# Kernel tuning notes

Measured on AMD Instinct MI355X. Metric: run time of the kernel, lower is better.

The kernel has to match this reference:

```python
import jax, jax.numpy as jnp
import numpy as np
import math

B = 8
LATENT = 1024
K_DIM = 128   # conv input channels / view dim k
M_DIM = 256   # attention feature dim m
N = 4096      # points_num // num_branch; attention seq len
EPS = 1e-5


def _bn(h, g, b, m, v):
    # inference-mode BatchNorm1d over [B, C, L]
    return (h - m[None, :, None]) * (g / jnp.sqrt(v + EPS))[None, :, None] + b[None, :, None]


def _conv(h, w, b):
    # Conv1d with kernel_size=1 == channel matmul: h [B,C,L], w [O,C]
    return jnp.einsum('bcl,oc->bol', h, w) + b[None, :, None]


def setup_inputs() -> dict:
    key = jax.random.key(0)
    ks = jax.random.split(key, 64)
    it = iter(range(64))

    def nrm(shape, scale=0.05):
        return jax.random.normal(ks[next(it)], shape, jnp.float32) * scale

    def pos(shape):
        return jax.random.uniform(ks[next(it)], shape, jnp.float32, 0.5, 1.5)

    d = {}
    d['x'] = jax.random.normal(ks[next(it)], (B, LATENT), jnp.float32)
    d['fc1_w'] = nrm((M_DIM * K_DIM, LATENT))
    d['fc1_b'] = nrm((M_DIM * K_DIM,))
    d['c1q_w'] = nrm((64, K_DIM)); d['c1q_b'] = nrm((64,))
    d['c2q_w'] = nrm((128, 64));   d['c2q_b'] = nrm((128,))
    d['c3q_w'] = nrm((N, 128));    d['c3q_b'] = nrm((N,))
    d['c3k_w'] = nrm((N, 128));    d['c3k_b'] = nrm((N,))
    d['c1v_w'] = nrm((64, K_DIM)); d['c1v_b'] = nrm((64,))
    d['c2v_w'] = nrm((128, 64));   d['c2v_b'] = nrm((128,))
    d['c3v_w'] = nrm((N, 128));    d['c3v_b'] = nrm((N,))
    for nm, c in [('bn1q', 64), ('bn2q', 128), ('bn1k', 64), ('bn2k', 128), ('bn1v', 64), ('bn2v', 128)]:
        d[nm + '_g'] = pos((c,))
        d[nm + '_be'] = nrm((c,))
        d[nm + '_m'] = nrm((c,))
        d[nm + '_v'] = pos((c,))
    d['co_w'] = nrm((3, M_DIM)); d['co_b'] = nrm((3,))
    return d


def _forward(x, fc1_w, fc1_b, c1q_w, c1q_b, c2q_w, c2q_b, c3q_w, c3q_b, c3k_w, c3k_b,
             c1v_w, c1v_b, c2v_w, c2v_b, c3v_w, c3v_b,
             bn1q_g, bn1q_be, bn1q_m, bn1q_v, bn2q_g, bn2q_be, bn2q_m, bn2q_v,
             bn1k_g, bn1k_be, bn1k_m, bn1k_v, bn2k_g, bn2k_be, bn2k_m, bn2k_v,
             bn1v_g, bn1v_be, bn1v_m, bn1v_v, bn2v_g, bn2v_be, bn2v_m, bn2v_v,
             co_w, co_b):
    h = (x @ fc1_w.T + fc1_b).reshape(-1, M_DIM, K_DIM)   # [B, m, k]
    h = jnp.transpose(h, (0, 2, 1))                        # [B, k, m]
    # Q path
    Q = jax.nn.relu(_bn(_conv(h, c1q_w, c1q_b), bn1q_g, bn1q_be, bn1q_m, bn1q_v))
    Q = jax.nn.relu(_bn(_conv(Q, c2q_w, c2q_b), bn2q_g, bn2q_be, bn2q_m, bn2q_v))
    Q = _conv(Q, c3q_w, c3q_b)                             # [B, n, m]
    # K path: source re-uses conv1_q / conv2_q weights (faithful to original)
    K = jax.nn.relu(_bn(_conv(h, c1q_w, c1q_b), bn1k_g, bn1k_be, bn1k_m, bn1k_v))
    K = jax.nn.relu(_bn(_conv(K, c2q_w, c2q_b), bn2k_g, bn2k_be, bn2k_m, bn2k_v))
    K = _conv(K, c3k_w, c3k_b)                             # [B, n, m]
    # V path
    V = jax.nn.relu(_bn(_conv(h, c1v_w, c1v_b), bn1v_g, bn1v_be, bn1v_m, bn1v_v))
    V = jax.nn.relu(_bn(_conv(V, c2v_w, c2v_b), bn2v_g, bn2v_be, bn2v_m, bn2v_v))
    V = _conv(V, c3v_w, c3v_b)                             # [B, n, m]
    # hand-rolled attention: scores [B, n, n] (source scales by sqrt(k))
    scores = jnp.einsum('bim,bjm->bij', Q, K) / math.sqrt(K_DIM)
    attn = jax.nn.softmax(scores, axis=2)
    out = jnp.einsum('bij,bjm->bim', attn, V)              # [B, n, m]
    out = jnp.einsum('bnm,om->bon', out, co_w) + co_b[None, :, None]  # [B, 3, n]
    return jnp.transpose(out, (0, 2, 1))                   # [B, n, 3]


def reference(x, fc1_w, fc1_b, c1q_w, c1q_b, c2q_w, c2q_b, c3q_w, c3q_b, c3k_w, c3k_b,
              c1v_w, c1v_b, c2v_w, c2v_b, c3v_w, c3v_b,
              bn1q_g, bn1q_be, bn1q_m, bn1q_v, bn2q_g, bn2q_be, bn2q_m, bn2q_v,
              bn1k_g, bn1k_be, bn1k_m, bn1k_v, bn2k_g, bn2k_be, bn2k_m, bn2k_v,
              bn1v_g, bn1v_be, bn1v_m, bn1v_v, bn2v_g, bn2v_be, bn2v_m, bn2v_v,
              co_w, co_b):
    return _forward(x, fc1_w, fc1_b, c1q_w, c1q_b, c2q_w, c2q_b, c3q_w, c3q_b, c3k_w, c3k_b,
                    c1v_w, c1v_b, c2v_w, c2v_b, c3v_w, c3v_b,
                    bn1q_g, bn1q_be, bn1q_m, bn1q_v, bn2q_g, bn2q_be, bn2q_m, bn2q_v,
                    bn1k_g, bn1k_be, bn1k_m, bn1k_v, bn2k_g, bn2k_be, bn2k_m, bn2k_v,
                    bn1v_g, bn1v_be, bn1v_m, bn1v_v, bn2v_g, bn2v_be, bn2v_m, bn2v_v,
                    co_w, co_b)
```

## Files before the change

kernel.cpp:

```cpp
#include <hip/hip_runtime.h>
#include <cstdint>
#include <cstddef>

#define EPS 1e-5f

typedef __attribute__((ext_vector_type(8))) short bf16x8;
typedef __attribute__((ext_vector_type(4))) float f32x4;
typedef __attribute__((ext_vector_type(16))) float f32x16;

__device__ __forceinline__ unsigned short rne_bf16(float f) {
  union { float f; unsigned int u; } v; v.f = f;
  unsigned int u = v.u;
  return (unsigned short)((u + 0x7fffu + ((u >> 16) & 1u)) >> 16);
}
__device__ __forceinline__ float bf16_to_f(unsigned short h) {
  union { unsigned int u; float f; } v; v.u = ((unsigned int)h) << 16; return v.f;
}
__device__ __forceinline__ void split_hl(float v, unsigned short& h, unsigned short& l) {
  h = rne_bf16(v);
  l = rne_bf16(v - bf16_to_f(h));
}
__device__ __forceinline__ f32x4 mfma16(bf16x8 a, bf16x8 b, f32x4 c) {
  return __builtin_amdgcn_mfma_f32_16x16x32_bf16(a, b, c, 0, 0, 0);
}
__device__ __forceinline__ f32x16 mfma32(bf16x8 a, bf16x8 b, f32x16 c) {
  return __builtin_amdgcn_mfma_f32_32x32x16_bf16(a, b, c, 0, 0, 0);
}

__global__ __launch_bounds__(256) void k_fc1(const float* __restrict__ x,
                                             const float* __restrict__ w,
                                             const float* __restrict__ bias,
                                             float* __restrict__ h_t) {
  const int lane = threadIdx.x & 63;
  const int wv = threadIdx.x >> 6;
  const int r = blockIdx.x * 4 + wv;
  const float4* wr = (const float4*)(w + (size_t)r * 1024);
  float acc[8] = {0, 0, 0, 0, 0, 0, 0, 0};
#pragma unroll
  for (int i = 0; i < 4; ++i) {
    float4 wv4 = wr[lane + i * 64];
#pragma unroll
    for (int b = 0; b < 8; ++b) {
      float4 xv = ((const float4*)(x + b * 1024))[lane + i * 64];
      acc[b] += wv4.x * xv.x + wv4.y * xv.y + wv4.z * xv.z + wv4.w * xv.w;
    }
  }
#pragma unroll
  for (int d = 1; d < 64; d <<= 1) {
#pragma unroll
    for (int b = 0; b < 8; ++b) acc[b] += __shfl_xor(acc[b], d);
  }
  if (lane == 0) {
    const int mm = r >> 7, kk = r & 127;
    const float bb = bias[r];
#pragma unroll
    for (int b = 0; b < 8; ++b) h_t[b * 32768 + kk * 256 + mm] = acc[b] + bb;
  }
}

__global__ __launch_bounds__(256) void k_conv1(
    const float* __restrict__ h_t,
    const float* __restrict__ c1q_w, const float* __restrict__ c1q_b,
    const float* __restrict__ c1v_w, const float* __restrict__ c1v_b,
    const float* __restrict__ g1q, const float* __restrict__ be1q,
    const float* __restrict__ mu1q, const float* __restrict__ va1q,
    const float* __restrict__ g1k, const float* __restrict__ be1k,
    const float* __restrict__ mu1k, const float* __restrict__ va1k,
    const float* __restrict__ g1v, const float* __restrict__ be1v,
    const float* __restrict__ mu1v, const float* __restrict__ va1v,
    float* __restrict__ T1q, float* __restrict__ T1k, float* __restrict__ T1v) {
  const int m = threadIdx.x;
  const int o = blockIdx.x & 63;
  const int b = blockIdx.x >> 6;
  const int path = blockIdx.y;
  const float* w = (path == 0 ? c1q_w : c1v_w) + o * 128;
  const float* h = h_t + b * 32768 + m;
  float acc = 0.f;
#pragma unroll 8
  for (int c = 0; c < 128; ++c) acc += w[c] * h[c * 256];
  if (path == 0) {
    const float z = acc + c1q_b[o];
    const float sq = g1q[o] / sqrtf(va1q[o] + EPS);
    T1q[b * 16384 + o * 256 + m] = fmaxf((z - mu1q[o]) * sq + be1q[o], 0.f);
    const float sk = g1k[o] / sqrtf(va1k[o] + EPS);
    T1k[b * 16384 + o * 256 + m] = fmaxf((z - mu1k[o]) * sk + be1k[o], 0.f);
  } else {
    const float z = acc + c1v_b[o];
    const float sv = g1v[o] / sqrtf(va1v[o] + EPS);
    T1v[b * 16384 + o * 256 + m] = fmaxf((z - mu1v[o]) * sv + be1v[o], 0.f);
  }
}

__global__ __launch_bounds__(256) void k_conv2(
    const float* __restrict__ T1q, const float* __restrict__ T1k,
    const float* __restrict__ T1v,
    const float* __restrict__ c2q_w, const float* __restrict__ c2q_b,
    const float* __restrict__ c2v_w, const float* __restrict__ c2v_b,
    const float* __restrict__ g2q, const float* __restrict__ be2q,
    const float* __restrict__ mu2q, const float* __restrict__ va2q,
    const float* __restrict__ g2k, const float* __restrict__ be2k,
    const float* __restrict__ mu2k, const float* __restrict__ va2k,
    const float* __restrict__ g2v, const float* __restrict__ be2v,
    const float* __restrict__ mu2v, const float* __restrict__ va2v,
    unsigned short* __restrict__ Q2H, unsigned short* __restrict__ Q2L,
    unsigned short* __restrict__ K2H, unsigned short* __restrict__ K2L,
    float* __restrict__ V2F) {
  const int m = threadIdx.x;
  const int b = blockIdx.x;
  const int path = blockIdx.y;
  const int oc = blockIdx.z;
  const float* T1 = (path == 0 ? T1q : path == 1 ? T1k : T1v) + b * 16384 + m;
  const float* w = (path == 2 ? c2v_w : c2q_w);
  const float* cb = (path == 2 ? c2v_b : c2q_b);
  const float* g = (path == 0 ? g2q : path == 1 ? g2k : g2v);
  const float* be = (path == 0 ? be2q : path == 1 ? be2k : be2v);
  const float* mu = (path == 0 ? mu2q : path == 1 ? mu2k : mu2v);
  const float* va = (path == 0 ? va2q : path == 1 ? va2k : va2v);
  float t[64];
#pragma unroll
  for (int c = 0; c < 64; ++c) t[c] = T1[c * 256];
  unsigned short* oh =
      (path == 0 ? Q2H : K2H) + b * 32768 + m * 128 + oc * 64;
  unsigned short* ol =
      (path == 0 ? Q2L : K2L) + b * 32768 + m * 128 + oc * 64;
  for (int og = 0; og < 8; ++og) {
    bf16x8 ph, pl;
#pragma unroll
    for (int j = 0; j < 8; ++j) {
      const int o = oc * 64 + og * 8 + j;
      float acc = cb[o];
      const float* wo = w + o * 64;
#pragma unroll
      for (int c = 0; c < 64; ++c) acc += wo[c] * t[c];
      const float s = g[o] / sqrtf(va[o] + EPS);
      const float val = fmaxf((acc - mu[o]) * s + be[o], 0.f);
      if (path == 2) {
        V2F[b * 32768 + o * 256 + m] = val;
      } else {
        unsigned short hh, ll;
        split_hl(val, hh, ll);
        ph[j] = (short)hh; pl[j] = (short)ll;
      }
    }
    if (path != 2) {
      *(bf16x8*)(oh + og * 8) = ph;
      *(bf16x8*)(ol + og * 8) = pl;
    }
  }
}

__global__ __launch_bounds__(256) void k_conv3all(
    const float* __restrict__ c3q_w, const float* __restrict__ c3q_b,
    const float* __restrict__ c3k_w, const float* __restrict__ c3k_b,
    const unsigned short* __restrict__ Q2H, const unsigned short* __restrict__ Q2L,
    const unsigned short* __restrict__ K2H, const unsigned short* __restrict__ K2L,
    unsigned short* __restrict__ QhB, unsigned short* __restrict__ QlB,
    unsigned short* __restrict__ KhB, unsigned short* __restrict__ KlB,
    const float* __restrict__ c3v_w, const float* __restrict__ c3v_b,
    const float* __restrict__ V2F, const float* __restrict__ co_w,
    float4* __restrict__ Vpp) {
  const int z = blockIdx.z;
  const int b = blockIdx.y;
  if (z == 2) {
    if (blockIdx.x >= 16) return;
    __shared__ float Us[387];
    __shared__ float Up[256][3];
    const int tt = threadIdx.x;
    {
      const int c = tt >> 1, mh = tt & 1;
      const float* v = V2F + b * 32768 + c * 256 + mh * 128;
      const float* cw0 = co_w + mh * 128;
      float u0 = 0.f, u1 = 0.f, u2 = 0.f;
#pragma unroll 4
      for (int mm = 0; mm < 128; ++mm) {
        const float xv = v[mm];
        u0 += xv * cw0[mm];
        u1 += xv * cw0[256 + mm];
        u2 += xv * cw0[512 + mm];
      }
      Up[tt][0] = u0; Up[tt][1] = u1; Up[tt][2] = u2;
      if (tt < 3) {
        float s = 0.f;
        for (int mm = 0; mm < 256; ++mm) s += co_w[tt * 256 + mm];
        Us[384 + tt] = s;
      }
    }
    __syncthreads();
    if ((tt & 1) == 0) {
      const int c = tt >> 1;
      Us[c * 3 + 0] = Up[tt][0] + Up[tt + 1][0];
      Us[c * 3 + 1] = Up[tt][1] + Up[tt + 1][1];
      Us[c * 3 + 2] = Up[tt][2] + Up[tt + 1][2];
    }
    __syncthreads();
    const int n = blockIdx.x * 256 + tt;
    const float* w = c3v_w + (size_t)n * 128;
    float a0 = 0.f, a1 = 0.f, a2 = 0.f;
#pragma unroll 4
    for (int c = 0; c < 128; ++c) {
      const float wc = w[c];
      a0 += wc * Us[c * 3 + 0];
      a1 += wc * Us[c * 3 + 1];
      a2 += wc * Us[c * 3 + 2];
    }
    const float bb = c3v_b[n];
    Vpp[(size_t)b * 4096 + n] =
        make_float4(a0 + bb * Us[384], a1 + bb * Us[385], a2 + bb * Us[386], 0.f);
    return;
  }
  const float* W = (z == 0) ? c3q_w : c3k_w;
  const float* bias = (z == 0) ? c3q_b : c3k_b;
  const unsigned short* Xh = (z == 0) ? Q2H : K2H;
  const unsigned short* Xl = (z == 0) ? Q2L : K2L;
  unsigned short* Yh = (z == 0) ? QhB : KhB;
  unsigned short* Yl = (z == 0) ? QlB : KlB;
  const float scale = (z == 0) ? 0.08838834764831845f * 1.4426950408889634f : 1.0f;
  const int lane = threadIdx.x & 63, wv = threadIdx.x >> 6;
  const int l15 = lane & 15, quad = lane >> 4;
  const unsigned short* XH = Xh + b * 32768;
  const unsigned short* XL = Xl + b * 32768;
  unsigned short* YH = Yh + (size_t)b * 4096 * 256;
  unsigned short* YL = Yl + (size_t)b * 4096 * 256;
  const int nb = blockIdx.x * 64 + wv * 16;
  const float* wr = W + (size_t)(nb + l15) * 128 + quad * 8;
  bf16x8 ah[4], al[4];
#pragma unroll
  for (int ks = 0; ks < 4; ++ks) {
#pragma unroll
    for (int j = 0; j < 8; ++j) {
      unsigned short hh, ll;
      split_hl(wr[ks * 32 + j], hh, ll);
      ah[ks][j] = (short)hh; al[ks][j] = (short)ll;
    }
  }
  f32x4 acc[16];
#pragma unroll
  for (int ms = 0; ms < 16; ++ms) acc[ms] = (f32x4){0, 0, 0, 0};
#pragma unroll
  for (int ks = 0; ks < 4; ++ks) {
#pragma unroll
    for (int ms = 0; ms < 16; ++ms) {
      const size_t off = (size_t)(ms * 16 + l15) * 128 + ks * 32 + quad * 8;
      bf16x8 bh = *(const bf16x8*)(XH + off);
      bf16x8 bl = *(const bf16x8*)(XL + off);
      acc[ms] = mfma16(ah[ks], bh, acc[ms]);
      acc[ms] = mfma16(al[ks], bh, acc[ms]);
      acc[ms] = mfma16(ah[ks], bl, acc[ms]);
    }
  }
#pragma unroll
  for (int r = 0; r < 4; ++r) {
    const int n = nb + quad * 4 + r;
    const float bv = bias[n];
#pragma unroll
    for (int ms = 0; ms < 16; ++ms) {
      const float v = (acc[ms][r] + bv) * scale;
      unsigned short hh, ll;
      split_hl(v, hh, ll);
      YH[(size_t)n * 256 + ms * 16 + l15] = hh;
      YL[(size_t)n * 256 + ms * 16 + l15] = ll;
    }
  }
}

__global__ __launch_bounds__(256, 2) void k_attn(
    const unsigned short* __restrict__ Qh, const unsigned short* __restrict__ Ql,
    const unsigned short* __restrict__ Kh, const unsigned short* __restrict__ Kl,
    const float4* __restrict__ Vpp, float4* __restrict__ part) {
  __shared__ __align__(16) short Kt[2][2][32 * 264];
  __shared__ __align__(16) float4 Vt[2][32];
  const int t = threadIdx.x;
  const int lane = t & 63, wv = t >> 6;
  const int l31 = lane & 31, half = lane >> 5;
  const int b = blockIdx.x & 7;
  const int qt = (blockIdx.x >> 3) & 31;
  const int jh = blockIdx.x >> 8;
  const int qrow = qt * 128 + wv * 32 + l31;
  const size_t qoff = ((size_t)b * 4096 + qrow) * 256 + half * 8;
  bf16x8 qfh[16], qfl[16];
#pragma unroll
  for (int kc = 0; kc < 16; ++kc) {
    qfh[kc] = *(const bf16x8*)(Qh + qoff + kc * 16);
    qfl[kc] = *(const bf16x8*)(Ql + qoff + kc * 16);
  }
  const unsigned short* Kgh = Kh + (size_t)b * 4096 * 256;
  const unsigned short* Kgl = Kl + (size_t)b * 4096 * 256;
  const float4* Vg = Vpp + (size_t)b * 4096;
  const int r0 = t >> 5;
  const int sseg = (t & 31) * 8;
  float a0 = 0.f, a1 = 0.f, a2 = 0.f, al = 0.f;
  const int jt0 = jh * 64;
  {
    const int jbase = jt0 * 32;
#pragma unroll
    for (int i = 0; i < 4; ++i) {
      const int row = i * 8 + r0;
      const size_t g = (size_t)(jbase + row) * 256 + sseg;
      *(bf16x8*)&Kt[0][0][row * 264 + sseg] = *(const bf16x8*)(Kgh + g);
      *(bf16x8*)&Kt[0][1][row * 264 + sseg] = *(const bf16x8*)(Kgl + g);
    }
    if (t < 32) Vt[0][t] = Vg[jbase + t];
  }
  __syncthreads();
  for (int it = 0; it < 64; ++it) {
    const int cur = it & 1, nxt = cur ^ 1;
    const bool pf = (it < 63);
    bf16x8 th[4], tl[4];
    float4 vpf = make_float4(0.f, 0.f, 0.f, 0.f);
    if (pf) {
      const int jb2 = (jt0 + it + 1) * 32;
#pragma unroll
      for (int i = 0; i < 4; ++i) {
        const size_t g = (size_t)(jb2 + i * 8 + r0) * 256 + sseg;
        th[i] = *(const bf16x8*)(Kgh + g);
        tl[i] = *(const bf16x8*)(Kgl + g);
      }
      if (t < 32) vpf = Vg[jb2 + t];
    }
    f32x16 sA, sB;
#pragma unroll
    for (int r = 0; r < 16; ++r) { sA[r] = 0.f; sB[r] = 0.f; }
    const short* KH = Kt[cur][0];
    const short* KL = Kt[cur][1];
#pragma unroll
    for (int kc = 0; kc < 16; ++kc) {
      bf16x8 kh = *(const bf16x8*)&KH[l31 * 264 + kc * 16 + half * 8];
      bf16x8 kl = *(const bf16x8*)&KL[l31 * 264 + kc * 16 + half * 8];
      sA = mfma32(kh, qfh[kc], sA);
      sB = mfma32(kh, qfl[kc], sB);
      sA = mfma32(kl, qfh[kc], sA);
    }
#pragma unroll
    for (int r = 0; r < 16; ++r) {
      const float p = __builtin_amdgcn_exp2f(sA[r] + sB[r]);
      const float4 vj = Vt[cur][(r & 3) + 8 * (r >> 2) + 4 * half];
      a0 += p * vj.x; a1 += p * vj.y; a2 += p * vj.z; al += p;
    }
    if (pf) {
#pragma unroll
      for (int i = 0; i < 4; ++i) {
        const int row = i * 8 + r0;
        *(bf16x8*)&Kt[nxt][0][row * 264 + sseg] = th[i];
        *(bf16x8*)&Kt[nxt][1][row * 264 + sseg] = tl[i];
      }
      if (t < 32) Vt[nxt][t] = vpf;
    }
    __syncthreads();
  }
  a0 += __shfl_xor(a0, 32);
  a1 += __shfl_xor(a1, 32);
  a2 += __shfl_xor(a2, 32);
  al += __shfl_xor(al, 32);
  if (half == 0)
    part[(size_t)jh * 32768 + (size_t)b * 4096 + qrow] =
        make_float4(a0, a1, a2, al);
}

__global__ __launch_bounds__(256) void k_combine(
    const float4* __restrict__ part, const float* __restrict__ co_b,
    float* __restrict__ out) {
  const int i = blockIdx.x * 256 + threadIdx.x;
  const float4 pa = part[i];
  const float4 pb = part[32768 + i];
  const float rl = 1.f / (pa.w + pb.w);
  const float b0 = co_b[0], b1 = co_b[1], b2 = co_b[2];
  out[(size_t)i * 3 + 0] = (pa.x + pb.x) * rl + b0;
  out[(size_t)i * 3 + 1] = (pa.y + pb.y) * rl + b1;
  out[(size_t)i * 3 + 2] = (pa.z + pb.z) * rl + b2;
}

extern "C" void kernel_launch(void* const* d_in, const int* in_sizes, int n_in,
                              void* d_out, int out_size, void* d_ws, size_t ws_size,
                              hipStream_t stream) {
  const float* x = (const float*)d_in[0];
  const float* fc1_w = (const float*)d_in[1];
  const float* fc1_b = (const float*)d_in[2];
  const float* c1q_w = (const float*)d_in[3];
  const float* c1q_b = (const float*)d_in[4];
  const float* c2q_w = (const float*)d_in[5];
  const float* c2q_b = (const float*)d_in[6];
  const float* c3q_w = (const float*)d_in[7];
  const float* c3q_b = (const float*)d_in[8];
  const float* c3k_w = (const float*)d_in[9];
  const float* c3k_b = (const float*)d_in[10];
  const float* c1v_w = (const float*)d_in[11];
  const float* c1v_b = (const float*)d_in[12];
  const float* c2v_w = (const float*)d_in[13];
  const float* c2v_b = (const float*)d_in[14];
  const float* c3v_w = (const float*)d_in[15];
  const float* c3v_b = (const float*)d_in[16];
  const float* bn1q_g = (const float*)d_in[17];
  const float* bn1q_be = (const float*)d_in[18];
  const float* bn1q_m = (const float*)d_in[19];
  const float* bn1q_v = (const float*)d_in[20];
  const float* bn2q_g = (const float*)d_in[21];
  const float* bn2q_be = (const float*)d_in[22];
  const float* bn2q_m = (const float*)d_in[23];
  const float* bn2q_v = (const float*)d_in[24];
  const float* bn1k_g = (const float*)d_in[25];
  const float* bn1k_be = (const float*)d_in[26];
  const float* bn1k_m = (const float*)d_in[27];
  const float* bn1k_v = (const float*)d_in[28];
  const float* bn2k_g = (const float*)d_in[29];
  const float* bn2k_be = (const float*)d_in[30];
  const float* bn2k_m = (const float*)d_in[31];
  const float* bn2k_v = (const float*)d_in[32];
  const float* bn1v_g = (const float*)d_in[33];
  const float* bn1v_be = (const float*)d_in[34];
  const float* bn1v_m = (const float*)d_in[35];
  const float* bn1v_v = (const float*)d_in[36];
  const float* bn2v_g = (const float*)d_in[37];
  const float* bn2v_be = (const float*)d_in[38];
  const float* bn2v_m = (const float*)d_in[39];
  const float* bn2v_v = (const float*)d_in[40];
  const float* co_w = (const float*)d_in[41];
  const float* co_b = (const float*)d_in[42];

  char* ws = (char*)d_ws;
  float* h_t = (float*)(ws + 0);
  float* T1q = (float*)(ws + 1048576);
  float* T1k = (float*)(ws + 1572864);
  float* T1v = (float*)(ws + 2097152);
  unsigned short* Q2H = (unsigned short*)(ws + 2621440);
  unsigned short* Q2L = (unsigned short*)(ws + 3145728);
  unsigned short* K2H = (unsigned short*)(ws + 3670016);
  unsigned short* K2L = (unsigned short*)(ws + 4194304);
  float* V2F = (float*)(ws + 4718592);
  unsigned short* QhB = (unsigned short*)(ws + 5767168);
  unsigned short* QlB = (unsigned short*)(ws + 22544384);
  unsigned short* KhB = (unsigned short*)(ws + 39321600);
  unsigned short* KlB = (unsigned short*)(ws + 56098816);
  float4* Vpp = (float4*)(ws + 72876032);
  float4* part = (float4*)(ws + 73416704);

  k_fc1<<<8192, 256, 0, stream>>>(x, fc1_w, fc1_b, h_t);
  k_conv1<<<dim3(512, 2), 256, 0, stream>>>(
      h_t, c1q_w, c1q_b, c1v_w, c1v_b,
      bn1q_g, bn1q_be, bn1q_m, bn1q_v,
      bn1k_g, bn1k_be, bn1k_m, bn1k_v,
      bn1v_g, bn1v_be, bn1v_m, bn1v_v,
      T1q, T1k, T1v);
  k_conv2<<<dim3(8, 3, 2), 256, 0, stream>>>(
      T1q, T1k, T1v, c2q_w, c2q_b, c2v_w, c2v_b,
      bn2q_g, bn2q_be, bn2q_m, bn2q_v,
      bn2k_g, bn2k_be, bn2k_m, bn2k_v,
      bn2v_g, bn2v_be, bn2v_m, bn2v_v,
      Q2H, Q2L, K2H, K2L, V2F);
  k_conv3all<<<dim3(64, 8, 3), 256, 0, stream>>>(
      c3q_w, c3q_b, c3k_w, c3k_b, Q2H, Q2L, K2H, K2L,
      QhB, QlB, KhB, KlB, c3v_w, c3v_b, V2F, co_w, Vpp);
  k_attn<<<512, 256, 0, stream>>>(QhB, QlB, KhB, KlB, Vpp, part);
  k_combine<<<128, 256, 0, stream>>>(part, co_b, (float*)d_out);
}
```

Before: 666.8 us.

## Split attention key range four ways with single-buffered LDS and higher occupancy

The attention kernel now splits the 4096 keys into four chunks instead of two, launching 1024 blocks. It drops the register-staged double buffering of K and V tiles in favour of a single LDS buffer guarded by two barriers per tile. It also raises the occupancy hint to four blocks per CU and gives the third MFMA chain its own accumulator so the chains are independent. The combine kernel sums four partials instead of two. The trade-off is that load/compute overlap now comes from other resident waves rather than prefetch, and the tighter register budget may cause spills given the large per-thread Q fragments.

Result: slower. 836.2 us (+25.4%).

```diff
diff --git a/kernel.cpp b/kernel.cpp
--- a/kernel.cpp
+++ b/kernel.cpp
@@ -263,18 +263,19 @@
   }
 }
 
-__global__ __launch_bounds__(256, 2) void k_attn(
+__global__ __launch_bounds__(256, 4) void k_attn(
     const unsigned short* __restrict__ Qh, const unsigned short* __restrict__ Ql,
     const unsigned short* __restrict__ Kh, const unsigned short* __restrict__ Kl,
     const float4* __restrict__ Vpp, float4* __restrict__ part) {
-  __shared__ __align__(16) short Kt[2][2][32 * 264];
-  __shared__ __align__(16) float4 Vt[2][32];
+  __shared__ __align__(16) short Kth[32 * 264];
+  __shared__ __align__(16) short Ktl[32 * 264];
+  __shared__ __align__(16) float4 Vt[32];
   const int t = threadIdx.x;
   const int lane = t & 63, wv = t >> 6;
   const int l31 = lane & 31, half = lane >> 5;
   const int b = blockIdx.x & 7;
   const int qt = (blockIdx.x >> 3) & 31;
-  const int jh = blockIdx.x >> 8;
+  const int jq = blockIdx.x >> 8;
   const int qrow = qt * 128 + wv * 32 + l31;
   const size_t qoff = ((size_t)b * 4096 + qrow) * 256 + half * 8;
   bf16x8 qfh[16], qfl[16];
@@ -289,70 +290,43 @@
   const int r0 = t >> 5;
   const int sseg = (t & 31) * 8;
   float a0 = 0.f, a1 = 0.f, a2 = 0.f, al = 0.f;
-  const int jt0 = jh * 64;
-  {
-    const int jbase = jt0 * 32;
+  const int jt0 = jq * 32;
+  for (int jt = jt0; jt < jt0 + 32; ++jt) {
+    const int jbase = jt * 32;
+    __syncthreads();
 #pragma unroll
     for (int i = 0; i < 4; ++i) {
       const int row = i * 8 + r0;
       const size_t g = (size_t)(jbase + row) * 256 + sseg;
-      *(bf16x8*)&Kt[0][0][row * 264 + sseg] = *(const bf16x8*)(Kgh + g);
-      *(bf16x8*)&Kt[0][1][row * 264 + sseg] = *(const bf16x8*)(Kgl + g);
-    }
-    if (t < 32) Vt[0][t] = Vg[jbase + t];
-  }
-  __syncthreads();
-  for (int it = 0; it < 64; ++it) {
-    const int cur = it & 1, nxt = cur ^ 1;
-    const bool pf = (it < 63);
-    bf16x8 th[4], tl[4];
-    float4 vpf = make_float4(0.f, 0.f, 0.f, 0.f);
-    if (pf) {
-      const int jb2 = (jt0 + it + 1) * 32;
-#pragma unroll
-      for (int i = 0; i < 4; ++i) {
-        const size_t g = (size_t)(jb2 + i * 8 + r0) * 256 + sseg;
-        th[i] = *(const bf16x8*)(Kgh + g);
-        tl[i] = *(const bf16x8*)(Kgl + g);
-      }
-      if (t < 32) vpf = Vg[jb2 + t];
-    }
-    f32x16 sA, sB;
-#pragma unroll
-    for (int r = 0; r < 16; ++r) { sA[r] = 0.f; sB[r] = 0.f; }
-    const short* KH = Kt[cur][0];
-    const short* KL = Kt[cur][1];
+      *(bf16x8*)&Kth[row * 264 + sseg] = *(const bf16x8*)(Kgh + g);
+      *(bf16x8*)&Ktl[row * 264 + sseg] = *(const bf16x8*)(Kgl + g);
+    }
+    if (t < 32) Vt[t] = Vg[jbase + t];
+    __syncthreads();
+    f32x16 sA, sB, sC;
+#pragma unroll
+    for (int r = 0; r < 16; ++r) { sA[r] = 0.f; sB[r] = 0.f; sC[r] = 0.f; }
 #pragma unroll
     for (int kc = 0; kc < 16; ++kc) {
-      bf16x8 kh = *(const bf16x8*)&KH[l31 * 264 + kc * 16 + half * 8];
-      bf16x8 kl = *(const bf16x8*)&KL[l31 * 264 + kc * 16 + half * 8];
+      bf16x8 kh = *(const bf16x8*)&Kth[l31 * 264 + kc * 16 + half * 8];
+      bf16x8 kl = *(const bf16x8*)&Ktl[l31 * 264 + kc * 16 + half * 8];
       sA = mfma32(kh, qfh[kc], sA);
       sB = mfma32(kh, qfl[kc], sB);
-      sA = mfma32(kl, qfh[kc], sA);
+      sC = mfma32(kl, qfh[kc], sC);
     }
 #pragma unroll
     for (int r = 0; r < 16; ++r) {
-      const float p = __builtin_amdgcn_exp2f(sA[r] + sB[r]);
-      const float4 vj = Vt[cur][(r & 3) + 8 * (r >> 2) + 4 * half];
+      const float p = __builtin_amdgcn_exp2f(sA[r] + sB[r] + sC[r]);
+      const float4 vj = Vt[(r & 3) + 8 * (r >> 2) + 4 * half];
       a0 += p * vj.x; a1 += p * vj.y; a2 += p * vj.z; al += p;
     }
-    if (pf) {
-#pragma unroll
-      for (int i = 0; i < 4; ++i) {
-        const int row = i * 8 + r0;
-        *(bf16x8*)&Kt[nxt][0][row * 264 + sseg] = th[i];
-        *(bf16x8*)&Kt[nxt][1][row * 264 + sseg] = tl[i];
-      }
-      if (t < 32) Vt[nxt][t] = vpf;
-    }
-    __syncthreads();
   }
   a0 += __shfl_xor(a0, 32);
   a1 += __shfl_xor(a1, 32);
   a2 += __shfl_xor(a2, 32);
   al += __shfl_xor(al, 32);
   if (half == 0)
-    part[(size_t)jh * 32768 + (size_t)b * 4096 + qrow] =
+    part[(size_t)jq * 32768 + (size_t)b * 4096 + qrow] =
         make_float4(a0, a1, a2, al);
 }
 
@@ -360,13 +334,14 @@
     const float4* __restrict__ part, const float* __restrict__ co_b,
     float* __restrict__ out) {
   const int i = blockIdx.x * 256 + threadIdx.x;
-  const float4 pa = part[i];
-  const float4 pb = part[32768 + i];
-  const float rl = 1.f / (pa.w + pb.w);
-  const float b0 = co_b[0], b1 = co_b[1], b2 = co_b[2];
-  out[(size_t)i * 3 + 0] = (pa.x + pb.x) * rl + b0;
-  out[(size_t)i * 3 + 1] = (pa.y + pb.y) * rl + b1;
-  out[(size_t)i * 3 + 2] = (pa.z + pb.z) * rl + b2;
+  const float4 p0 = part[i];
+  const float4 p1 = part[32768 + i];
+  const float4 p2 = part[65536 + i];
+  const float4 p3 = part[98304 + i];
+  const float rl = 1.f / (p0.w + p1.w + p2.w + p3.w);
+  out[(size_t)i * 3 + 0] = (p0.x + p1.x + p2.x + p3.x) * rl + co_b[0];
+  out[(size_t)i * 3 + 1] = (p0.y + p1.y + p2.y + p3.y) * rl + co_b[1];
+  out[(size_t)i * 3 + 2] = (p0.z + p1.z + p2.z + p3.z) * rl + co_b[2];
 }
 
 extern "C" void kernel_launch(void* const* d_in, const int* in_sizes, int n_in,
@@ -449,6 +424,6 @@
   k_conv3all<<<dim3(64, 8, 3), 256, 0, stream>>>(
       c3q_w, c3q_b, c3k_w, c3k_b, Q2H, Q2L, K2H, K2L,
       QhB, QlB, KhB, KlB, c3v_w, c3v_b, V2F, co_w, Vpp);
-  k_attn<<<512, 256, 0, stream>>>(QhB, QlB, KhB, KlB, Vpp, part);
+  k_attn<<<1024, 256, 0, stream>>>(QhB, QlB, KhB, KlB, Vpp, part);
   k_combine<<<128, 256, 0, stream>>>(part, co_b, (float*)d_out);
 }
```
